# Performance work log

Hardware: AMD Instinct MI355X
Metric: run time of the kernel (lower is better)

Reference implementation:

```python
import jax, jax.numpy as jnp
import numpy as np

B, S, H = 2, 2048, 1024
NH, NKV, HD = 16, 4, 64
E, K, I = 8, 2, 2048
EPS = 1e-6
THETA = 10000.0


def rmsnorm(x, w):
    v = jnp.mean(jnp.square(x.astype(jnp.float32)), axis=-1, keepdims=True)
    return (x.astype(jnp.float32) * jax.lax.rsqrt(v + EPS)).astype(x.dtype) * w


def apply_rope(q, k, pos):
    # q: [B,S,NH,HD], k: [B,S,NKV,HD], pos: [B,S]
    inv_freq = 1.0 / (THETA ** (jnp.arange(0, HD, 2, dtype=jnp.float32) / HD))
    ang = pos.astype(jnp.float32)[..., None] * inv_freq          # [B,S,HD/2]
    emb = jnp.concatenate([ang, ang], axis=-1)                   # [B,S,HD]
    cos = jnp.cos(emb)[:, :, None, :]
    sin = jnp.sin(emb)[:, :, None, :]

    def rot(x):
        return jnp.concatenate([-x[..., HD // 2:], x[..., :HD // 2]], axis=-1)

    q = (q * cos + rot(q) * sin).astype(q.dtype)
    k = (k * cos + rot(k) * sin).astype(k.dtype)
    return q, k


def setup_inputs() -> dict:
    key = jax.random.key(0)
    ks = jax.random.split(key, 10)
    sc = 0.02
    return dict(
        hidden_states=jax.random.normal(ks[0], (B, S, H), jnp.float32),
        attention_mask=jnp.ones((B, S), jnp.int32),
        position_ids=jnp.broadcast_to(jnp.arange(S, dtype=jnp.int32), (B, S)),
        norm1_w=jnp.ones((H,), jnp.float32),
        norm2_w=jnp.ones((H,), jnp.float32),
        wq=jax.random.normal(ks[1], (H, NH * HD), jnp.float32) * sc,
        wk=jax.random.normal(ks[2], (H, NKV * HD), jnp.float32) * sc,
        wv=jax.random.normal(ks[3], (H, NKV * HD), jnp.float32) * sc,
        wo=jax.random.normal(ks[4], (NH * HD, H), jnp.float32) * sc,
        gate_w=jax.random.normal(ks[5], (H, E), jnp.float32) * sc,
        w1=jax.random.normal(ks[6], (E, H, I), jnp.float32) * sc,
        w3=jax.random.normal(ks[7], (E, H, I), jnp.float32) * sc,
        w2=jax.random.normal(ks[8], (E, I, H), jnp.float32) * sc,
    )


def reference(hidden_states, attention_mask, position_ids, norm1_w, norm2_w,
              wq, wk, wv, wo, gate_w, w1, w3, w2):
    x = hidden_states
    # --- attention block ---
    h = rmsnorm(x, norm1_w)
    q = (h @ wq).reshape(B, S, NH, HD)
    k = (h @ wk).reshape(B, S, NKV, HD)
    v = (h @ wv).reshape(B, S, NKV, HD)
    q, k = apply_rope(q, k, position_ids)
    rep = NH // NKV
    k = jnp.repeat(k, rep, axis=2)   # [B,S,NH,HD]
    v = jnp.repeat(v, rep, axis=2)
    q = q.transpose(0, 2, 1, 3)      # [B,NH,S,HD]
    k = k.transpose(0, 2, 1, 3)
    v = v.transpose(0, 2, 1, 3)
    scores = jnp.einsum('bhqd,bhkd->bhqk', q, k) / jnp.sqrt(jnp.float32(HD))
    causal = jnp.tril(jnp.ones((S, S), jnp.bool_))
    mask = causal[None, None, :, :] & (attention_mask[:, None, None, :] > 0)
    neg = jnp.finfo(jnp.float32).min
    scores = jnp.where(mask, scores, neg)
    attn = jax.nn.softmax(scores.astype(jnp.float32), axis=-1).astype(x.dtype)
    o = jnp.einsum('bhqk,bhkd->bhqd', attn, v)
    o = o.transpose(0, 2, 1, 3).reshape(B, S, NH * HD) @ wo
    x = x + o
    # --- MoE block ---
    h = rmsnorm(x, norm2_w)
    router_logits = (h @ gate_w).astype(jnp.float32)            # [B,S,E]
    routing_weights, selected_experts = jax.lax.top_k(router_logits, K)
    routing_weights = jax.nn.softmax(routing_weights, axis=-1)  # [B,S,K]
    moe = jnp.zeros_like(h)
    for e in range(E):
        eo = (jax.nn.silu(h @ w1[e]) * (h @ w3[e])) @ w2[e]     # [B,S,H]
        wgt = jnp.sum((selected_experts == e) * routing_weights, axis=-1)[:, :, None]
        moe = moe + wgt.astype(h.dtype) * eo
    x = x + moe
    return x, router_logits
```

## Files before the change

kernel.cpp:

```cpp
#include <hip/hip_runtime.h>
#include <cstdint>
#include <cstddef>

#define BB 2
#define SS 2048
#define HH 1024
#define NHEADS 16
#define NKVH 4
#define HDIM 64
#define NEXP 8
#define IDIM 2048
#define NTOK (BB*SS)

typedef __bf16 bf16_t;
typedef bf16_t bf16x8 __attribute__((ext_vector_type(8)));
typedef bf16_t bf16x4 __attribute__((ext_vector_type(4)));
typedef float f32x4 __attribute__((ext_vector_type(4)));

static __device__ __forceinline__ void gl16(const void* g, void* l) {
  __builtin_amdgcn_global_load_lds(
      (const __attribute__((address_space(1))) unsigned int*)g,
      (__attribute__((address_space(3))) unsigned int*)l, 16, 0, 0);
}

__global__ __launch_bounds__(256) void transpose_cvt(
    const float* __restrict__ W, bf16_t* __restrict__ WT, int K, int N)
{
  const float* Wm = W + (size_t)blockIdx.z * K * N;
  bf16_t* Tm = WT + (size_t)blockIdx.z * K * N;
  __shared__ float Ls[64][65];
  int tid = threadIdx.x;
  int k0 = blockIdx.y * 64, n0 = blockIdx.x * 64;
  int rr = tid >> 4, cc = (tid & 15) * 4;
  #pragma unroll
  for (int rep = 0; rep < 4; ++rep) {
    float4 vv = *(const float4*)(Wm + (size_t)(k0 + rep*16 + rr) * N + n0 + cc);
    Ls[rep*16 + rr][cc+0] = vv.x;
    Ls[rep*16 + rr][cc+1] = vv.y;
    Ls[rep*16 + rr][cc+2] = vv.z;
    Ls[rep*16 + rr][cc+3] = vv.w;
  }
  __syncthreads();
  int nn = tid >> 2, ks = (tid & 3) * 16;
  bf16x8 o0, o1;
  #pragma unroll
  for (int j = 0; j < 8; ++j) o0[j] = (bf16_t)Ls[ks + j][nn];
  #pragma unroll
  for (int j = 0; j < 8; ++j) o1[j] = (bf16_t)Ls[ks + 8 + j][nn];
  bf16_t* op = Tm + (size_t)(n0 + nn) * K + k0 + ks;
  *(bf16x8*)op = o0;
  *(bf16x8*)(op + 8) = o1;
}

__global__ __launch_bounds__(256) void rmsnorm_kernel(
    const float* __restrict__ x, const float* __restrict__ w,
    float* __restrict__ outf, bf16_t* __restrict__ outb)
{
  int t = blockIdx.x;
  int tid = threadIdx.x;
  float4 v = ((const float4*)(x + (size_t)t * HH))[tid];
  float ss = v.x*v.x + v.y*v.y + v.z*v.z + v.w*v.w;
  #pragma unroll
  for (int off = 32; off > 0; off >>= 1) ss += __shfl_xor(ss, off);
  __shared__ float red[4];
  if ((tid & 63) == 0) red[tid >> 6] = ss;
  __syncthreads();
  float tot = red[0] + red[1] + red[2] + red[3];
  float scale = 1.0f / sqrtf(tot / (float)HH + 1e-6f);
  float4 wv = ((const float4*)w)[tid];
  float4 o;
  o.x = v.x * scale * wv.x;
  o.y = v.y * scale * wv.y;
  o.z = v.z * scale * wv.z;
  o.w = v.w * scale * wv.w;
  if (outf) ((float4*)(outf + (size_t)t * HH))[tid] = o;
  bf16x4 ob4 = { (bf16_t)o.x, (bf16_t)o.y, (bf16_t)o.z, (bf16_t)o.w };
  *(bf16x4*)(outb + (size_t)t * HH + tid*4) = ob4;
}

__global__ __launch_bounds__(256) void gemm_bt(
    const bf16_t* __restrict__ A, const bf16_t* __restrict__ Bt,
    const float* __restrict__ R, float* __restrict__ C, int N, int K)
{
  __shared__ __align__(16) bf16_t As[4096];
  __shared__ __align__(16) bf16_t Bs[4096];
  int tid = threadIdx.x, lane = tid & 63, w = tid >> 6;
  int l4 = lane & 15, g = lane >> 4;
  int m0 = blockIdx.y * 128, n0 = blockIdx.x * 128;
  int lrow = w*16 + (lane >> 2), lk = (lane & 3) * 8;
  const bf16_t* ag0 = A + (size_t)(m0 + lrow) * K + lk;
  const bf16_t* ag1 = ag0 + (size_t)64 * K;
  const bf16_t* bg0 = Bt + (size_t)(n0 + lrow) * K + lk;
  const bf16_t* bg1 = bg0 + (size_t)64 * K;
  bf16_t* lA0 = As + w*512;  bf16_t* lA1 = As + 2048 + w*512;
  bf16_t* lB0 = Bs + w*512;  bf16_t* lB1 = Bs + 2048 + w*512;
  const f32x4 fz = {0.f,0.f,0.f,0.f};
  f32x4 acc[4][4];
  #pragma unroll
  for (int i = 0; i < 4; ++i) { acc[i][0]=fz; acc[i][1]=fz; acc[i][2]=fz; acc[i][3]=fz; }
  int wm = (w >> 1) * 64, wn = (w & 1) * 64;
  for (int k0 = 0; k0 < K; k0 += 32) {
    __syncthreads();
    gl16(ag0, lA0); gl16(ag1, lA1); gl16(bg0, lB0); gl16(bg1, lB1);
    ag0 += 32; ag1 += 32; bg0 += 32; bg1 += 32;
    __syncthreads();
    bf16x8 af[4], bfr[4];
    #pragma unroll
    for (int mi = 0; mi < 4; ++mi) af[mi] = *(const bf16x8*)&As[(wm + mi*16 + l4)*32 + g*8];
    #pragma unroll
    for (int ni = 0; ni < 4; ++ni) bfr[ni] = *(const bf16x8*)&Bs[(wn + ni*16 + l4)*32 + g*8];
    #pragma unroll
    for (int mi = 0; mi < 4; ++mi)
      #pragma unroll
      for (int ni = 0; ni < 4; ++ni)
        acc[mi][ni] = __builtin_amdgcn_mfma_f32_16x16x32_bf16(af[mi], bfr[ni], acc[mi][ni], 0, 0, 0);
  }
  #pragma unroll
  for (int mi = 0; mi < 4; ++mi) {
    int rowb = m0 + wm + mi*16 + g*4;
    #pragma unroll
    for (int r = 0; r < 4; ++r) {
      size_t rb = (size_t)(rowb + r) * N;
      #pragma unroll
      for (int ni = 0; ni < 4; ++ni) {
        int col = n0 + wn + ni*16 + l4;
        float vv = acc[mi][ni][r];
        C[rb + col] = R ? vv + R[rb + col] : vv;
      }
    }
  }
}

__global__ __launch_bounds__(256) void rope_kernel(
    float* __restrict__ q, float* __restrict__ k, const int* __restrict__ pos_ids)
{
  int idx = blockIdx.x * 256 + threadIdx.x;
  int token = idx / 640;
  int rem = idx - token * 640;
  int head = rem >> 5;
  int i = rem & 31;
  float pos = (float)pos_ids[token];
  float inv = __expf(-(float)i * (9.210340371976184f / 32.0f));
  float ang = pos * inv;
  float s, c;
  sincosf(ang, &s, &c);
  float* p;
  if (head < NHEADS) p = q + (size_t)token * (NHEADS*HDIM) + head * HDIM;
  else               p = k + (size_t)token * (NKVH*HDIM) + (head - NHEADS) * HDIM;
  float x1 = p[i], x2 = p[i + 32];
  p[i]      = x1 * c - x2 * s;
  p[i + 32] = x2 * c + x1 * s;
}

__global__ __launch_bounds__(256) void attn_mfma_kernel(
    const float* __restrict__ q, const float* __restrict__ k, const float* __restrict__ v,
    const int* __restrict__ amask, bf16_t* __restrict__ out)
{
  __shared__ bf16_t Khi[64][72];
  __shared__ bf16_t Klo[64][72];
  __shared__ bf16_t Vhi[64][72];
  __shared__ bf16_t Vlo[64][72];
  __shared__ bf16_t Phi[4][16][72];
  __shared__ bf16_t Plo[4][16][72];
  __shared__ float ms[64];
  int tid = threadIdx.x, lane = tid & 63, w = tid >> 6;
  int l4 = lane & 15, g = lane >> 4;
  int bh = blockIdx.y;
  int b = bh >> 4, h = bh & 15, kvh = h >> 2;
  int qb = gridDim.x - 1 - blockIdx.x;
  int r0 = qb * 64;

  bf16x8 qh[2], ql[2];
  {
    const float* qp = q + (size_t)(b*SS + r0 + w*16 + l4) * (NHEADS*HDIM) + h*HDIM + g*8;
    #pragma unroll
    for (int st = 0; st < 2; ++st) {
      float4 t0 = *(const float4*)(qp + st*32);
      float4 t1 = *(const float4*)(qp + st*32 + 4);
      float f[8] = {t0.x*0.125f, t0.y*0.125f, t0.z*0.125f, t0.w*0.125f,
                    t1.x*0.125f, t1.y*0.125f, t1.z*0.125f, t1.w*0.125f};
      #pragma unroll
      for (int j = 0; j < 8; ++j) {
        bf16_t hi = (bf16_t)f[j];
        qh[st][j] = hi;
        ql[st][j] = (bf16_t)(f[j] - (float)hi);
      }
    }
  }
  const f32x4 fz = {0.f,0.f,0.f,0.f};
  f32x4 o[4]; o[0]=fz; o[1]=fz; o[2]=fz; o[3]=fz;
  float mrow[4] = {-3e38f,-3e38f,-3e38f,-3e38f};
  float lrow[4] = {0.f,0.f,0.f,0.f};

  int vkey = tid & 63;
  int dvb = (tid >> 6) * 16;
  int nch = qb + 1;
  for (int ch = 0; ch < nch; ++ch) {
    int kc = ch * 64;
    __syncthreads();
    #pragma unroll
    for (int it = 0; it < 4; ++it) {
      int slot = it*256 + tid;
      int key = slot >> 4, dq = (slot & 15) * 4;
      float4 kk4 = *(const float4*)(k + (size_t)(b*SS + kc + key)*(NKVH*HDIM) + kvh*HDIM + dq);
      bf16_t kh0 = (bf16_t)kk4.x, kh1 = (bf16_t)kk4.y, kh2 = (bf16_t)kk4.z, kh3 = (bf16_t)kk4.w;
      bf16x4 khv = {kh0, kh1, kh2, kh3};
      bf16x4 klv = { (bf16_t)(kk4.x-(float)kh0), (bf16_t)(kk4.y-(float)kh1),
                     (bf16_t)(kk4.z-(float)kh2), (bf16_t)(kk4.w-(float)kh3) };
      *(bf16x4*)&Khi[key][dq] = khv;
      *(bf16x4*)&Klo[key][dq] = klv;
      int dv = dvb + it*4;
      float4 vv4 = *(const float4*)(v + (size_t)(b*SS + kc + vkey)*(NKVH*HDIM) + kvh*HDIM + dv);
      float vf4[4] = {vv4.x, vv4.y, vv4.z, vv4.w};
      #pragma unroll
      for (int j = 0; j < 4; ++j) {
        bf16_t hi = (bf16_t)vf4[j];
        Vhi[dv+j][vkey] = hi;
        Vlo[dv+j][vkey] = (bf16_t)(vf4[j] - (float)hi);
      }
    }
    if (tid < 64) ms[tid] = (amask[b*SS + kc + tid] > 0) ? 0.f : -3e38f;
    __syncthreads();
    f32x4 s[4]; s[0]=fz; s[1]=fz; s[2]=fz; s[3]=fz;
    #pragma unroll
    for (int st = 0; st < 2; ++st) {
      #pragma unroll
      for (int c = 0; c < 4; ++c) {
        bf16x8 kfh = *(const bf16x8*)&Khi[c*16 + l4][st*32 + g*8];
        bf16x8 kfl = *(const bf16x8*)&Klo[c*16 + l4][st*32 + g*8];
        s[c] = __builtin_amdgcn_mfma_f32_16x16x32_bf16(qh[st], kfh, s[c], 0, 0, 0);
        s[c] = __builtin_amdgcn_mfma_f32_16x16x32_bf16(qh[st], kfl, s[c], 0, 0, 0);
        s[c] = __builtin_amdgcn_mfma_f32_16x16x32_bf16(ql[st], kfh, s[c], 0, 0, 0);
      }
    }
    #pragma unroll
    for (int c = 0; c < 4; ++c) {
      int kg = kc + c*16 + l4;
      float mk = ms[c*16 + l4];
      #pragma unroll
      for (int r = 0; r < 4; ++r) {
        int rowg = r0 + w*16 + g*4 + r;
        float sv = s[c][r] + mk;
        s[c][r] = (kg <= rowg) ? sv : -3e38f;
      }
    }
    float mnew[4], alpha[4];
    #pragma unroll
    for (int r = 0; r < 4; ++r) {
      float mc = fmaxf(fmaxf(s[0][r], s[1][r]), fmaxf(s[2][r], s[3][r]));
      mc = fmaxf(mc, __shfl_xor(mc, 1));
      mc = fmaxf(mc, __shfl_xor(mc, 2));
      mc = fmaxf(mc, __shfl_xor(mc, 4));
      mc = fmaxf(mc, __shfl_xor(mc, 8));
      mnew[r] = fmaxf(mrow[r], mc);
      alpha[r] = __expf(mrow[r] - mnew[r]);
      mrow[r] = mnew[r];
    }
    float rsum[4] = {0.f,0.f,0.f,0.f};
    #pragma unroll
    for (int c = 0; c < 4; ++c) {
      #pragma unroll
      for (int r = 0; r < 4; ++r) {
        float p = __expf(s[c][r] - mnew[r]);
        s[c][r] = p;
        rsum[r] += p;
      }
    }
    #pragma unroll
    for (int r = 0; r < 4; ++r) {
      float t = rsum[r];
      t += __shfl_xor(t, 1); t += __shfl_xor(t, 2);
      t += __shfl_xor(t, 4); t += __shfl_xor(t, 8);
      lrow[r] = lrow[r] * alpha[r] + t;
      o[0][r] *= alpha[r]; o[1][r] *= alpha[r]; o[2][r] *= alpha[r]; o[3][r] *= alpha[r];
    }
    #pragma unroll
    for (int c = 0; c < 4; ++c) {
      #pragma unroll
      for (int r = 0; r < 4; ++r) {
        float p = s[c][r];
        bf16_t hi = (bf16_t)p;
        Phi[w][g*4 + r][c*16 + l4] = hi;
        Plo[w][g*4 + r][c*16 + l4] = (bf16_t)(p - (float)hi);
      }
    }
    __syncthreads();
    #pragma unroll
    for (int st = 0; st < 2; ++st) {
      bf16x8 pfh = *(const bf16x8*)&Phi[w][l4][st*32 + g*8];
      bf16x8 pfl = *(const bf16x8*)&Plo[w][l4][st*32 + g*8];
      #pragma unroll
      for (int c = 0; c < 4; ++c) {
        bf16x8 vfh = *(const bf16x8*)&Vhi[c*16 + l4][st*32 + g*8];
        bf16x8 vfl = *(const bf16x8*)&Vlo[c*16 + l4][st*32 + g*8];
        o[c] = __builtin_amdgcn_mfma_f32_16x16x32_bf16(pfh, vfh, o[c], 0, 0, 0);
        o[c] = __builtin_amdgcn_mfma_f32_16x16x32_bf16(pfl, vfh, o[c], 0, 0, 0);
        o[c] = __builtin_amdgcn_mfma_f32_16x16x32_bf16(pfh, vfl, o[c], 0, 0, 0);
      }
    }
  }
  #pragma unroll
  for (int r = 0; r < 4; ++r) {
    float inv = (lrow[r] > 0.f) ? 1.f / lrow[r] : 0.f;
    int row = r0 + w*16 + g*4 + r;
    bf16_t* op = out + (size_t)(b*SS + row) * (NHEADS*HDIM) + h*HDIM;
    #pragma unroll
    for (int c = 0; c < 4; ++c)
      op[c*16 + l4] = (bf16_t)(o[c][r] * inv);
  }
}

__global__ __launch_bounds__(256) void router_kernel(
    const float* __restrict__ h2, const float* __restrict__ gw,
    float* __restrict__ logits_out, int* __restrict__ sel, float* __restrict__ wts,
    int* __restrict__ counts)
{
  int tid = threadIdx.x, lane = tid & 63, w = tid >> 6;
  int tok = blockIdx.x * 4 + w;
  float acc[NEXP] = {0.f,0.f,0.f,0.f,0.f,0.f,0.f,0.f};
  const float* xr = h2 + (size_t)tok * HH;
  for (int hh = lane; hh < HH; hh += 64) {
    float xv = xr[hh];
    const float* gr = gw + (size_t)hh * NEXP;
    #pragma unroll
    for (int e = 0; e < NEXP; ++e) acc[e] += xv * gr[e];
  }
  #pragma unroll
  for (int e = 0; e < NEXP; ++e) {
    #pragma unroll
    for (int off = 32; off > 0; off >>= 1) acc[e] += __shfl_xor(acc[e], off);
  }
  if (lane == 0) {
    float* lo = logits_out + (size_t)tok * NEXP;
    #pragma unroll
    for (int e = 0; e < NEXP; ++e) lo[e] = acc[e];
    int b0 = 0; float v0 = acc[0];
    #pragma unroll
    for (int e = 1; e < NEXP; ++e) if (acc[e] > v0) { v0 = acc[e]; b0 = e; }
    int b1 = -1; float v1 = -1e38f;
    #pragma unroll
    for (int e = 0; e < NEXP; ++e) if (e != b0 && acc[e] > v1) { v1 = acc[e]; b1 = e; }
    float wa = 1.f / (1.f + __expf(v1 - v0));
    sel[tok*2] = b0; sel[tok*2+1] = b1;
    wts[tok*2] = wa; wts[tok*2+1] = 1.f - wa;
    atomicAdd(&counts[b0], 1);
    atomicAdd(&counts[b1], 1);
  }
}

__global__ void scan_kernel(const int* __restrict__ counts, int* __restrict__ offsets,
                            int* __restrict__ fill)
{
  if (threadIdx.x == 0 && blockIdx.x == 0) {
    int o = 0;
    for (int e = 0; e < NEXP; ++e) { offsets[e] = o; o += counts[e]; fill[e] = 0; }
  }
}

__global__ __launch_bounds__(256) void scatter_kernel(
    const int* __restrict__ sel, const int* __restrict__ offsets, int* __restrict__ fill,
    int* __restrict__ etok, int* __restrict__ tslot)
{
  int t = blockIdx.x * 256 + threadIdx.x;
  if (t >= NTOK) return;
  #pragma unroll
  for (int s = 0; s < 2; ++s) {
    int e = sel[t*2 + s];
    int p = atomicAdd(&fill[e], 1);
    int slot = offsets[e] + p;
    etok[slot] = t;
    tslot[t*2 + s] = slot;
  }
}

__global__ __launch_bounds__(256) void moe_mm1(
    const bf16_t* __restrict__ hb, const bf16_t* __restrict__ w1t,
    const int* __restrict__ counts, const int* __restrict__ offsets,
    const int* __restrict__ etok, bf16_t* __restrict__ G)
{
  int e = blockIdx.z, cnt = counts[e], mb = blockIdx.y;
  if (mb * 128 >= cnt) return;
  int off = offsets[e];
  __shared__ __align__(16) bf16_t As[4096];
  __shared__ __align__(16) bf16_t Bs[4096];
  int tid = threadIdx.x, lane = tid & 63, w = tid >> 6;
  int l4 = lane & 15, g = lane >> 4;
  int n0 = blockIdx.x * 128;
  int lrow = w*16 + (lane >> 2), lk = (lane & 3) * 8;
  int r0 = mb*128 + lrow, r1 = r0 + 64;
  int t0 = etok[off + (r0 < cnt ? r0 : cnt-1)];
  int t1 = etok[off + (r1 < cnt ? r1 : cnt-1)];
  const bf16_t* ag0 = hb + (size_t)t0 * HH + lk;
  const bf16_t* ag1 = hb + (size_t)t1 * HH + lk;
  const bf16_t* Bt = w1t + (size_t)e * IDIM * HH;
  const bf16_t* bg0 = Bt + (size_t)(n0 + lrow) * HH + lk;
  const bf16_t* bg1 = bg0 + (size_t)64 * HH;
  bf16_t* lA0 = As + w*512;  bf16_t* lA1 = As + 2048 + w*512;
  bf16_t* lB0 = Bs + w*512;  bf16_t* lB1 = Bs + 2048 + w*512;
  const f32x4 fz = {0.f,0.f,0.f,0.f};
  f32x4 acc[4][4];
  #pragma unroll
  for (int i = 0; i < 4; ++i) { acc[i][0]=fz; acc[i][1]=fz; acc[i][2]=fz; acc[i][3]=fz; }
  int wm = (w >> 1) * 64, wn = (w & 1) * 64;
  for (int k0 = 0; k0 < HH; k0 += 32) {
    __syncthreads();
    gl16(ag0, lA0); gl16(ag1, lA1); gl16(bg0, lB0); gl16(bg1, lB1);
    ag0 += 32; ag1 += 32; bg0 += 32; bg1 += 32;
    __syncthreads();
    bf16x8 af[4], bfr[4];
    #pragma unroll
    for (int mi = 0; mi < 4; ++mi) af[mi] = *(const bf16x8*)&As[(wm + mi*16 + l4)*32 + g*8];
    #pragma unroll
    for (int ni = 0; ni < 4; ++ni) bfr[ni] = *(const bf16x8*)&Bs[(wn + ni*16 + l4)*32 + g*8];
    #pragma unroll
    for (int mi = 0; mi < 4; ++mi)
      #pragma unroll
      for (int ni = 0; ni < 4; ++ni)
        acc[mi][ni] = __builtin_amdgcn_mfma_f32_16x16x32_bf16(af[mi], bfr[ni], acc[mi][ni], 0, 0, 0);
  }
  #pragma unroll
  for (int mi = 0; mi < 4; ++mi) {
    #pragma unroll
    for (int r = 0; r < 4; ++r) {
      int slot = mb*128 + wm + mi*16 + g*4 + r;
      if (slot < cnt) {
        size_t rb = (size_t)(off + slot) * IDIM;
        #pragma unroll
        for (int ni = 0; ni < 4; ++ni)
          G[rb + n0 + wn + ni*16 + l4] = (bf16_t)acc[mi][ni][r];
      }
    }
  }
}

__global__ __launch_bounds__(256) void moe_mm3(
    const bf16_t* __restrict__ hb, const bf16_t* __restrict__ w3t,
    const int* __restrict__ counts, const int* __restrict__ offsets,
    const int* __restrict__ etok, bf16_t* __restrict__ G)
{
  int e = blockIdx.z, cnt = counts[e], mb = blockIdx.y;
  if (mb * 128 >= cnt) return;
  int off = offsets[e];
  __shared__ __align__(16) bf16_t As[4096];
  __shared__ __align__(16) bf16_t Bs[4096];
  int tid = threadIdx.x, lane = tid & 63, w = tid >> 6;
  int l4 = lane & 15, g = lane >> 4;
  int n0 = blockIdx.x * 128;
  int lrow = w*16 + (lane >> 2), lk = (lane & 3) * 8;
  int r0 = mb*128 + lrow, r1 = r0 + 64;
  int t0 = etok[off + (r0 < cnt ? r0 : cnt-1)];
  int t1 = etok[off + (r1 < cnt ? r1 : cnt-1)];
  const bf16_t* ag0 = hb + (size_t)t0 * HH + lk;
  const bf16_t* ag1 = hb + (size_t)t1 * HH + lk;
  const bf16_t* Bt = w3t + (size_t)e * IDIM * HH;
  const bf16_t* bg0 = Bt + (size_t)(n0 + lrow) * HH + lk;
  const bf16_t* bg1 = bg0 + (size_t)64 * HH;
  bf16_t* lA0 = As + w*512;  bf16_t* lA1 = As + 2048 + w*512;
  bf16_t* lB0 = Bs + w*512;  bf16_t* lB1 = Bs + 2048 + w*512;
  const f32x4 fz = {0.f,0.f,0.f,0.f};
  f32x4 acc[4][4];
  #pragma unroll
  for (int i = 0; i < 4; ++i) { acc[i][0]=fz; acc[i][1]=fz; acc[i][2]=fz; acc[i][3]=fz; }
  int wm = (w >> 1) * 64, wn = (w & 1) * 64;
  for (int k0 = 0; k0 < HH; k0 += 32) {
    __syncthreads();
    gl16(ag0, lA0); gl16(ag1, lA1); gl16(bg0, lB0); gl16(bg1, lB1);
    ag0 += 32; ag1 += 32; bg0 += 32; bg1 += 32;
    __syncthreads();
    bf16x8 af[4], bfr[4];
    #pragma unroll
    for (int mi = 0; mi < 4; ++mi) af[mi] = *(const bf16x8*)&As[(wm + mi*16 + l4)*32 + g*8];
    #pragma unroll
    for (int ni = 0; ni < 4; ++ni) bfr[ni] = *(const bf16x8*)&Bs[(wn + ni*16 + l4)*32 + g*8];
    #pragma unroll
    for (int mi = 0; mi < 4; ++mi)
      #pragma unroll
      for (int ni = 0; ni < 4; ++ni)
        acc[mi][ni] = __builtin_amdgcn_mfma_f32_16x16x32_bf16(af[mi], bfr[ni], acc[mi][ni], 0, 0, 0);
  }
  #pragma unroll
  for (int mi = 0; mi < 4; ++mi) {
    #pragma unroll
    for (int r = 0; r < 4; ++r) {
      int slot = mb*128 + wm + mi*16 + g*4 + r;
      if (slot < cnt) {
        size_t rb = (size_t)(off + slot) * IDIM;
        #pragma unroll
        for (int ni = 0; ni < 4; ++ni) {
          size_t idx = rb + n0 + wn + ni*16 + l4;
          float gv = (float)G[idx];
          float sv = gv / (1.f + __expf(-gv));
          G[idx] = (bf16_t)(sv * acc[mi][ni][r]);
        }
      }
    }
  }
}

__global__ __launch_bounds__(256) void moe_mm2(
    const bf16_t* __restrict__ act, const bf16_t* __restrict__ w2t,
    const int* __restrict__ counts, const int* __restrict__ offsets,
    float* __restrict__ eo)
{
  int e = blockIdx.z, cnt = counts[e], mb = blockIdx.y;
  if (mb * 128 >= cnt) return;
  int off = offsets[e];
  __shared__ __align__(16) bf16_t As[4096];
  __shared__ __align__(16) bf16_t Bs[4096];
  int tid = threadIdx.x, lane = tid & 63, w = tid >> 6;
  int l4 = lane & 15, g = lane >> 4;
  int n0 = blockIdx.x * 128;
  int lrow = w*16 + (lane >> 2), lk = (lane & 3) * 8;
  int r0 = mb*128 + lrow, r1 = r0 + 64;
  int cr0 = (r0 < cnt ? r0 : cnt-1), cr1 = (r1 < cnt ? r1 : cnt-1);
  const bf16_t* ag0 = act + (size_t)(off + cr0) * IDIM + lk;
  const bf16_t* ag1 = act + (size_t)(off + cr1) * IDIM + lk;
  const bf16_t* Bt = w2t + (size_t)e * HH * IDIM;
  const bf16_t* bg0 = Bt + (size_t)(n0 + lrow) * IDIM + lk;
  const bf16_t* bg1 = bg0 + (size_t)64 * IDIM;
  bf16_t* lA0 = As + w*512;  bf16_t* lA1 = As + 2048 + w*512;
  bf16_t* lB0 = Bs + w*512;  bf16_t* lB1 = Bs + 2048 + w*512;
  const f32x4 fz = {0.f,0.f,0.f,0.f};
  f32x4 acc[4][4];
  #pragma unroll
  for (int i = 0; i < 4; ++i) { acc[i][0]=fz; acc[i][1]=fz; acc[i][2]=fz; acc[i][3]=fz; }
  int wm = (w >> 1) * 64, wn = (w & 1) * 64;
  for (int k0 = 0; k0 < IDIM; k0 += 32) {
    __syncthreads();
    gl16(ag0, lA0); gl16(ag1, lA1); gl16(bg0, lB0); gl16(bg1, lB1);
    ag0 += 32; ag1 += 32; bg0 += 32; bg1 += 32;
    __syncthreads();
    bf16x8 af[4], bfr[4];
    #pragma unroll
    for (int mi = 0; mi < 4; ++mi) af[mi] = *(const bf16x8*)&As[(wm + mi*16 + l4)*32 + g*8];
    #pragma unroll
    for (int ni = 0; ni < 4; ++ni) bfr[ni] = *(const bf16x8*)&Bs[(wn + ni*16 + l4)*32 + g*8];
    #pragma unroll
    for (int mi = 0; mi < 4; ++mi)
      #pragma unroll
      for (int ni = 0; ni < 4; ++ni)
        acc[mi][ni] = __builtin_amdgcn_mfma_f32_16x16x32_bf16(af[mi], bfr[ni], acc[mi][ni], 0, 0, 0);
  }
  #pragma unroll
  for (int mi = 0; mi < 4; ++mi) {
    #pragma unroll
    for (int r = 0; r < 4; ++r) {
      int slot = mb*128 + wm + mi*16 + g*4 + r;
      if (slot < cnt) {
        size_t rb = (size_t)(off + slot) * HH;
        #pragma unroll
        for (int ni = 0; ni < 4; ++ni)
          eo[rb + n0 + wn + ni*16 + l4] = acc[mi][ni][r];
      }
    }
  }
}

__global__ __launch_bounds__(256) void combine_kernel(
    const float* __restrict__ eo, const int* __restrict__ tslot,
    const float* __restrict__ wts, float* __restrict__ out)
{
  int t = blockIdx.x;
  int c = threadIdx.x * 4;
  int s0 = tslot[t*2], s1 = tslot[t*2 + 1];
  float w0 = wts[t*2], w1 = wts[t*2 + 1];
  float4 o = *(float4*)(out + (size_t)t * HH + c);
  float4 a = *(const float4*)(eo + (size_t)s0 * HH + c);
  float4 b = *(const float4*)(eo + (size_t)s1 * HH + c);
  o.x += w0*a.x + w1*b.x;
  o.y += w0*a.y + w1*b.y;
  o.z += w0*a.z + w1*b.z;
  o.w += w0*a.w + w1*b.w;
  *(float4*)(out + (size_t)t * HH + c) = o;
}

extern "C" void kernel_launch(void* const* d_in, const int* in_sizes, int n_in,
                              void* d_out, int out_size, void* d_ws, size_t ws_size,
                              hipStream_t stream)
{
  const float* x    = (const float*)d_in[0];
  const int*   am   = (const int*)d_in[1];
  const int*   pid  = (const int*)d_in[2];
  const float* n1w  = (const float*)d_in[3];
  const float* n2w  = (const float*)d_in[4];
  const float* wq   = (const float*)d_in[5];
  const float* wk   = (const float*)d_in[6];
  const float* wv   = (const float*)d_in[7];
  const float* wo   = (const float*)d_in[8];
  const float* gw   = (const float*)d_in[9];
  const float* w1   = (const float*)d_in[10];
  const float* w3   = (const float*)d_in[11];
  const float* w2   = (const float*)d_in[12];
  float* out = (float*)d_out;
  float* rlogits = out + (size_t)NTOK * HH;

  char* base = (char*)d_ws;
  bf16_t* hb  = (bf16_t*)(base);
  float*  h2  = (float*)(base + (8ull<<20));
  float*  qb  = (float*)(base + (24ull<<20));
  float*  kb  = (float*)(base + (40ull<<20));
  float*  vb  = (float*)(base + (44ull<<20));
  bf16_t* ob  = (bf16_t*)(base + (48ull<<20));
  bf16_t* G   = (bf16_t*)(base + (24ull<<20));
  float*  eo  = (float*)(base + (56ull<<20));
  bf16_t* wqt = (bf16_t*)(base + (88ull<<20));
  bf16_t* wkt = (bf16_t*)(base + (90ull<<20));
  bf16_t* wvt = (bf16_t*)(base + (90ull<<20) + (512ull<<10));
  bf16_t* wot = (bf16_t*)(base + (91ull<<20));
  bf16_t* w1t = (bf16_t*)(base + (93ull<<20));
  bf16_t* w3t = (bf16_t*)(base + (125ull<<20));
  bf16_t* w2t = (bf16_t*)(base + (157ull<<20));
  char* sm = base + (189ull<<20);
  int*   sel   = (int*)sm;
  float* wts   = (float*)(sm + (64<<10));
  int*   etok  = (int*)(sm + (128<<10));
  int*   tslot = (int*)(sm + (192<<10));
  int* counts  = (int*)(sm + (256<<10));
  int* offsets = counts + 8;
  int* fill    = counts + 16;

  transpose_cvt<<<dim3(16,16,1), 256, 0, stream>>>(wq, wqt, 1024, 1024);
  transpose_cvt<<<dim3(4,16,1),  256, 0, stream>>>(wk, wkt, 1024, 256);
  transpose_cvt<<<dim3(4,16,1),  256, 0, stream>>>(wv, wvt, 1024, 256);
  transpose_cvt<<<dim3(16,16,1), 256, 0, stream>>>(wo, wot, 1024, 1024);
  transpose_cvt<<<dim3(32,16,8), 256, 0, stream>>>(w1, w1t, 1024, 2048);
  transpose_cvt<<<dim3(32,16,8), 256, 0, stream>>>(w3, w3t, 1024, 2048);
  transpose_cvt<<<dim3(16,32,8), 256, 0, stream>>>(w2, w2t, 2048, 1024);
  hipMemsetAsync(counts, 0, 3 * 8 * sizeof(int), stream);

  rmsnorm_kernel<<<NTOK, 256, 0, stream>>>(x, n1w, nullptr, hb);
  gemm_bt<<<dim3(8,32),  256, 0, stream>>>(hb, wqt, nullptr, qb, NHEADS*HDIM, HH);
  gemm_bt<<<dim3(2,32),  256, 0, stream>>>(hb, wkt, nullptr, kb, NKVH*HDIM, HH);
  gemm_bt<<<dim3(2,32),  256, 0, stream>>>(hb, wvt, nullptr, vb, NKVH*HDIM, HH);
  rope_kernel<<<(NTOK*640)/256, 256, 0, stream>>>(qb, kb, pid);
  attn_mfma_kernel<<<dim3(SS/64, BB*NHEADS), 256, 0, stream>>>(qb, kb, vb, am, ob);
  gemm_bt<<<dim3(8,32),  256, 0, stream>>>(ob, wot, x, out, HH, NHEADS*HDIM);

  rmsnorm_kernel<<<NTOK, 256, 0, stream>>>(out, n2w, h2, hb);
  router_kernel<<<NTOK/4, 256, 0, stream>>>(h2, gw, rlogits, sel, wts, counts);
  scan_kernel<<<1, 64, 0, stream>>>(counts, offsets, fill);
  scatter_kernel<<<NTOK/256, 256, 0, stream>>>(sel, offsets, fill, etok, tslot);
  moe_mm1<<<dim3(16,32,8), 256, 0, stream>>>(hb, w1t, counts, offsets, etok, G);
  moe_mm3<<<dim3(16,32,8), 256, 0, stream>>>(hb, w3t, counts, offsets, etok, G);
  moe_mm2<<<dim3(8,32,8),  256, 0, stream>>>(G, w2t, counts, offsets, eo);
  combine_kernel<<<NTOK, 256, 0, stream>>>(eo, tslot, wts, out);
}
```

Before: 1.026 ms.

## Pre-pack K/V into swizzled bf16 hi/lo and use 128-row query tiles

A new pack_kv kernel converts K and V once into split bf16 hi/lo arrays, with V transposed and XOR-swizzled. The attention kernel can then load them straight into LDS with global_load_lds rather than converting them per block. Each attention block now covers 128 query rows across two 64-row sub-tiles, so every K/V chunk in LDS is reused twice. Fully masked causal sub-tiles are skipped, and launch bounds request 3 blocks per CU. The cost is an extra kernel launch, more registers per thread and fewer blocks in the grid. The __syncthreads between the P writes and P reads is also gone, since each wave uses only its own P buffer.

```diff
diff --git a/kernel.cpp b/kernel.cpp
--- a/kernel.cpp
+++ b/kernel.cpp
@@ -152,27 +152,78 @@
   p[i + 32] = x2 * c + x1 * s;
 }
 
-__global__ __launch_bounds__(256) void attn_mfma_kernel(
-    const float* __restrict__ q, const float* __restrict__ k, const float* __restrict__ v,
+__global__ __launch_bounds__(256) void pack_kv(
+    const float* __restrict__ kb, const float* __restrict__ vb,
+    bf16_t* __restrict__ Khig, bf16_t* __restrict__ Klog,
+    bf16_t* __restrict__ Vhig, bf16_t* __restrict__ Vlog)
+{
+  __shared__ float Ls[64][68];
+  int ch = blockIdx.x, bk = blockIdx.y;
+  int b = bk >> 2, kvh = bk & 3;
+  int tid = threadIdx.x;
+  int key = tid >> 2, d0 = (tid & 3) * 16;
+  size_t src = ((size_t)(b*SS + ch*64 + key) * NKVH + kvh) * HDIM + d0;
+  float f[16];
+  *(float4*)(f)     = *(const float4*)(kb + src);
+  *(float4*)(f+4)   = *(const float4*)(kb + src + 4);
+  *(float4*)(f+8)   = *(const float4*)(kb + src + 8);
+  *(float4*)(f+12)  = *(const float4*)(kb + src + 12);
+  size_t krow = ((size_t)bk*SS + ch*64 + key) * 64;
+  int sw = key & 7, j0 = d0 >> 3;
+  bf16x8 hi0, lo0, hi1, lo1;
+  #pragma unroll
+  for (int j = 0; j < 8; ++j) {
+    bf16_t h = (bf16_t)f[j];     hi0[j] = h; lo0[j] = (bf16_t)(f[j]   - (float)h);
+    bf16_t h2 = (bf16_t)f[8+j];  hi1[j] = h2; lo1[j] = (bf16_t)(f[8+j] - (float)h2);
+  }
+  *(bf16x8*)&Khig[krow + ((j0 ^ sw) << 3)]       = hi0;
+  *(bf16x8*)&Khig[krow + (((j0+1) ^ sw) << 3)]   = hi1;
+  *(bf16x8*)&Klog[krow + ((j0 ^ sw) << 3)]       = lo0;
+  *(bf16x8*)&Klog[krow + (((j0+1) ^ sw) << 3)]   = lo1;
+  *(float4*)&Ls[key][d0]      = *(const float4*)(vb + src);
+  *(float4*)&Ls[key][d0 + 4]  = *(const float4*)(vb + src + 4);
+  *(float4*)&Ls[key][d0 + 8]  = *(const float4*)(vb + src + 8);
+  *(float4*)&Ls[key][d0 + 12] = *(const float4*)(vb + src + 12);
+  __syncthreads();
+  int d = tid >> 2, k0 = (tid & 3) * 16;
+  size_t vrow = ((size_t)(bk*32 + ch) * 64 + d) * 64;
+  int swv = d & 7;
+  #pragma unroll
+  for (int half = 0; half < 2; ++half) {
+    bf16x8 vh, vl;
+    #pragma unroll
+    for (int j = 0; j < 8; ++j) {
+      float x = Ls[k0 + half*8 + j][d];
+      bf16_t h = (bf16_t)x;
+      vh[j] = h; vl[j] = (bf16_t)(x - (float)h);
+    }
+    int jj = (k0 >> 3) + half;
+    *(bf16x8*)&Vhig[vrow + ((jj ^ swv) << 3)] = vh;
+    *(bf16x8*)&Vlog[vrow + ((jj ^ swv) << 3)] = vl;
+  }
+}
+
+__global__ __launch_bounds__(256, 3) void attn_mfma_kernel(
+    const float* __restrict__ q,
+    const bf16_t* __restrict__ Khig, const bf16_t* __restrict__ Klog,
+    const bf16_t* __restrict__ Vhig, const bf16_t* __restrict__ Vlog,
     const int* __restrict__ amask, bf16_t* __restrict__ out)
 {
-  __shared__ bf16_t Khi[64][72];
-  __shared__ bf16_t Klo[64][72];
-  __shared__ bf16_t Vhi[64][72];
-  __shared__ bf16_t Vlo[64][72];
-  __shared__ bf16_t Phi[4][16][72];
-  __shared__ bf16_t Plo[4][16][72];
+  __shared__ __align__(16) bf16_t Khi[4096], Klo[4096], Vhi[4096], Vlo[4096];
+  __shared__ bf16_t Phi[4][16][72], Plo[4][16][72];
   __shared__ float ms[64];
   int tid = threadIdx.x, lane = tid & 63, w = tid >> 6;
   int l4 = lane & 15, g = lane >> 4;
   int bh = blockIdx.y;
   int b = bh >> 4, h = bh & 15, kvh = h >> 2;
+  int bk = b * NKVH + kvh;
   int qb = gridDim.x - 1 - blockIdx.x;
-  int r0 = qb * 64;
-
-  bf16x8 qh[2], ql[2];
-  {
-    const float* qp = q + (size_t)(b*SS + r0 + w*16 + l4) * (NHEADS*HDIM) + h*HDIM + g*8;
+  int r0 = qb * 128;
+
+  bf16x8 qh[2][2], ql[2][2];
+  #pragma unroll
+  for (int mi = 0; mi < 2; ++mi) {
+    const float* qp = q + (size_t)(b*SS + r0 + mi*64 + w*16 + l4) * (NHEADS*HDIM) + h*HDIM + g*8;
     #pragma unroll
     for (int st = 0; st < 2; ++st) {
       float4 t0 = *(const float4*)(qp + st*32);
@@ -182,131 +233,137 @@
       #pragma unroll
       for (int j = 0; j < 8; ++j) {
         bf16_t hi = (bf16_t)f[j];
-        qh[st][j] = hi;
-        ql[st][j] = (bf16_t)(f[j] - (float)hi);
+        qh[mi][st][j] = hi;
+        ql[mi][st][j] = (bf16_t)(f[j] - (float)hi);
       }
     }
   }
   const f32x4 fz = {0.f,0.f,0.f,0.f};
-  f32x4 o[4]; o[0]=fz; o[1]=fz; o[2]=fz; o[3]=fz;
-  float mrow[4] = {-3e38f,-3e38f,-3e38f,-3e38f};
-  float lrow[4] = {0.f,0.f,0.f,0.f};
-
-  int vkey = tid & 63;
-  int dvb = (tid >> 6) * 16;
-  int nch = qb + 1;
+  f32x4 o[2][4];
+  float mrow[2][4], lrow[2][4];
+  #pragma unroll
+  for (int mi = 0; mi < 2; ++mi)
+    #pragma unroll
+    for (int c = 0; c < 4; ++c) { o[mi][c] = fz; mrow[mi][c] = -3e38f; lrow[mi][c] = 0.f; }
+
+  const bf16_t* Khb = Khig + (size_t)bk*SS*64;
+  const bf16_t* Klb = Klog + (size_t)bk*SS*64;
+  const bf16_t* Vhb = Vhig + (size_t)bk*SS*64;
+  const bf16_t* Vlb = Vlog + (size_t)bk*SS*64;
+  int nch = 2*qb + 2;
   for (int ch = 0; ch < nch; ++ch) {
     int kc = ch * 64;
     __syncthreads();
-    #pragma unroll
-    for (int it = 0; it < 4; ++it) {
-      int slot = it*256 + tid;
-      int key = slot >> 4, dq = (slot & 15) * 4;
-      float4 kk4 = *(const float4*)(k + (size_t)(b*SS + kc + key)*(NKVH*HDIM) + kvh*HDIM + dq);
-      bf16_t kh0 = (bf16_t)kk4.x, kh1 = (bf16_t)kk4.y, kh2 = (bf16_t)kk4.z, kh3 = (bf16_t)kk4.w;
-      bf16x4 khv = {kh0, kh1, kh2, kh3};
-      bf16x4 klv = { (bf16_t)(kk4.x-(float)kh0), (bf16_t)(kk4.y-(float)kh1),
-                     (bf16_t)(kk4.z-(float)kh2), (bf16_t)(kk4.w-(float)kh3) };
-      *(bf16x4*)&Khi[key][dq] = khv;
-      *(bf16x4*)&Klo[key][dq] = klv;
-      int dv = dvb + it*4;
-      float4 vv4 = *(const float4*)(v + (size_t)(b*SS + kc + vkey)*(NKVH*HDIM) + kvh*HDIM + dv);
-      float vf4[4] = {vv4.x, vv4.y, vv4.z, vv4.w};
-      #pragma unroll
-      for (int j = 0; j < 4; ++j) {
-        bf16_t hi = (bf16_t)vf4[j];
-        Vhi[dv+j][vkey] = hi;
-        Vlo[dv+j][vkey] = (bf16_t)(vf4[j] - (float)hi);
-      }
+    {
+      size_t ko = (size_t)(kc + w*16) * 64 + lane*8;
+      gl16(Khb + ko,       Khi + w*1024);
+      gl16(Khb + ko + 512, Khi + w*1024 + 512);
+      gl16(Klb + ko,       Klo + w*1024);
+      gl16(Klb + ko + 512, Klo + w*1024 + 512);
+      size_t vo = (size_t)ch*4096 + (size_t)(w*16)*64 + lane*8;
+      gl16(Vhb + vo,       Vhi + w*1024);
+      gl16(Vhb + vo + 512, Vhi + w*1024 + 512);
+      gl16(Vlb + vo,       Vlo + w*1024);
+      gl16(Vlb + vo + 512, Vlo + w*1024 + 512);
     }
     if (tid < 64) ms[tid] = (amask[b*SS + kc + tid] > 0) ? 0.f : -3e38f;
     __syncthreads();
-    f32x4 s[4]; s[0]=fz; s[1]=fz; s[2]=fz; s[3]=fz;
-    #pragma unroll
-    for (int st = 0; st < 2; ++st) {
+    #pragma unroll
+    for (int mi = 0; mi < 2; ++mi) {
+      int tbase = r0 + mi*64 + w*16;
+      if (kc > tbase + 15) continue;
+      f32x4 s[4]; s[0]=fz; s[1]=fz; s[2]=fz; s[3]=fz;
+      #pragma unroll
+      for (int st = 0; st < 2; ++st) {
+        #pragma unroll
+        for (int c = 0; c < 4; ++c) {
+          int po = (c*16 + l4)*64 + (((st*4 + g) ^ (l4 & 7)) << 3);
+          bf16x8 kfh = *(const bf16x8*)&Khi[po];
+          bf16x8 kfl = *(const bf16x8*)&Klo[po];
+          s[c] = __builtin_amdgcn_mfma_f32_16x16x32_bf16(qh[mi][st], kfh, s[c], 0, 0, 0);
+          s[c] = __builtin_amdgcn_mfma_f32_16x16x32_bf16(qh[mi][st], kfl, s[c], 0, 0, 0);
+          s[c] = __builtin_amdgcn_mfma_f32_16x16x32_bf16(ql[mi][st], kfh, s[c], 0, 0, 0);
+        }
+      }
       #pragma unroll
       for (int c = 0; c < 4; ++c) {
-        bf16x8 kfh = *(const bf16x8*)&Khi[c*16 + l4][st*32 + g*8];
-        bf16x8 kfl = *(const bf16x8*)&Klo[c*16 + l4][st*32 + g*8];
-        s[c] = __builtin_amdgcn_mfma_f32_16x16x32_bf16(qh[st], kfh, s[c], 0, 0, 0);
-        s[c] = __builtin_amdgcn_mfma_f32_16x16x32_bf16(qh[st], kfl, s[c], 0, 0, 0);
-        s[c] = __builtin_amdgcn_mfma_f32_16x16x32_bf16(ql[st], kfh, s[c], 0, 0, 0);
-      }
-    }
-    #pragma unroll
-    for (int c = 0; c < 4; ++c) {
-      int kg = kc + c*16 + l4;
-      float mk = ms[c*16 + l4];
+        int kg = kc + c*16 + l4;
+        float mk = ms[c*16 + l4];
+        #pragma unroll
+        for (int r = 0; r < 4; ++r) {
+          int rowg = tbase + g*4 + r;
+          float sv = s[c][r] + mk;
+          s[c][r] = (kg <= rowg) ? sv : -3e38f;
+        }
+      }
+      float mnew[4], alpha[4];
       #pragma unroll
       for (int r = 0; r < 4; ++r) {
-        int rowg = r0 + w*16 + g*4 + r;
-        float sv = s[c][r] + mk;
-        s[c][r] = (kg <= rowg) ? sv : -3e38f;
-      }
-    }
-    float mnew[4], alpha[4];
+        float mc = fmaxf(fmaxf(s[0][r], s[1][r]), fmaxf(s[2][r], s[3][r]));
+        mc = fmaxf(mc, __shfl_xor(mc, 1));
+        mc = fmaxf(mc, __shfl_xor(mc, 2));
+        mc = fmaxf(mc, __shfl_xor(mc, 4));
+        mc = fmaxf(mc, __shfl_xor(mc, 8));
+        mnew[r] = fmaxf(mrow[mi][r], mc);
+        alpha[r] = __expf(mrow[mi][r] - mnew[r]);
+        mrow[mi][r] = mnew[r];
+      }
+      float rsum[4] = {0.f,0.f,0.f,0.f};
+      #pragma unroll
+      for (int c = 0; c < 4; ++c) {
+        #pragma unroll
+        for (int r = 0; r < 4; ++r) {
+          float p = __expf(s[c][r] - mnew[r]);
+          s[c][r] = p;
+          rsum[r] += p;
+        }
+      }
+      #pragma unroll
+      for (int r = 0; r < 4; ++r) {
+        float t = rsum[r];
+        t += __shfl_xor(t, 1); t += __shfl_xor(t, 2);
+        t += __shfl_xor(t, 4); t += __shfl_xor(t, 8);
+        lrow[mi][r] = lrow[mi][r] * alpha[r] + t;
+        o[mi][0][r] *= alpha[r]; o[mi][1][r] *= alpha[r];
+        o[mi][2][r] *= alpha[r]; o[mi][3][r] *= alpha[r];
+      }
+      #pragma unroll
+      for (int c = 0; c < 4; ++c) {
+        #pragma unroll
+        for (int r = 0; r < 4; ++r) {
+          float p = s[c][r];
+          bf16_t hi = (bf16_t)p;
+          Phi[w][g*4 + r][c*16 + l4] = hi;
+          Plo[w][g*4 + r][c*16 + l4] = (bf16_t)(p - (float)hi);
+        }
+      }
+      #pragma unroll
+      for (int st = 0; st < 2; ++st) {
+        bf16x8 pfh = *(const bf16x8*)&Phi[w][l4][st*32 + g*8];
+        bf16x8 pfl = *(const bf16x8*)&Plo[w][l4][st*32 + g*8];
+        #pragma unroll
+        for (int c = 0; c < 4; ++c) {
+          int po = (c*16 + l4)*64 + (((st*4 + g) ^ (l4 & 7)) << 3);
+          bf16x8 vfh = *(const bf16x8*)&Vhi[po];
+          bf16x8 vfl = *(const bf16x8*)&Vlo[po];
+          o[mi][c] = __builtin_amdgcn_mfma_f32_16x16x32_bf16(pfh, vfh, o[mi][c], 0, 0, 0);
+          o[mi][c] = __builtin_amdgcn_mfma_f32_16x16x32_bf16(pfl, vfh, o[mi][c], 0, 0, 0);
+          o[mi][c] = __builtin_amdgcn_mfma_f32_16x16x32_bf16(pfh, vfl, o[mi][c], 0, 0, 0);
+        }
+      }
+    }
+  }
+  #pragma unroll
+  for (int mi = 0; mi < 2; ++mi) {
     #pragma unroll
     for (int r = 0; r < 4; ++r) {
-      float mc = fmaxf(fmaxf(s[0][r], s[1][r]), fmaxf(s[2][r], s[3][r]));
-      mc = fmaxf(mc, __shfl_xor(mc, 1));
-      mc = fmaxf(mc, __shfl_xor(mc, 2));
-      mc = fmaxf(mc, __shfl_xor(mc, 4));
-      mc = fmaxf(mc, __shfl_xor(mc, 8));
-      mnew[r] = fmaxf(mrow[r], mc);
-      alpha[r] = __expf(mrow[r] - mnew[r]);
-      mrow[r] = mnew[r];
-    }
-    float rsum[4] = {0.f,0.f,0.f,0.f};
-    #pragma unroll
-    for (int c = 0; c < 4; ++c) {
-      #pragma unroll
-      for (int r = 0; r < 4; ++r) {
-        float p = __expf(s[c][r] - mnew[r]);
-        s[c][r] = p;
-        rsum[r] += p;
-      }
-    }
-    #pragma unroll
-    for (int r = 0; r < 4; ++r) {
-      float t = rsum[r];
-      t += __shfl_xor(t, 1); t += __shfl_xor(t, 2);
-      t += __shfl_xor(t, 4); t += __shfl_xor(t, 8);
-      lrow[r] = lrow[r] * alpha[r] + t;
-      o[0][r] *= alpha[r]; o[1][r] *= alpha[r]; o[2][r] *= alpha[r]; o[3][r] *= alpha[r];
-    }
-    #pragma unroll
-    for (int c = 0; c < 4; ++c) {
-      #pragma unroll
-      for (int r = 0; r < 4; ++r) {
-        float p = s[c][r];
-        bf16_t hi = (bf16_t)p;
-        Phi[w][g*4 + r][c*16 + l4] = hi;
-        Plo[w][g*4 + r][c*16 + l4] = (bf16_t)(p - (float)hi);
-      }
-    }
-    __syncthreads();
-    #pragma unroll
-    for (int st = 0; st < 2; ++st) {
-      bf16x8 pfh = *(const bf16x8*)&Phi[w][l4][st*32 + g*8];
-      bf16x8 pfl = *(const bf16x8*)&Plo[w][l4][st*32 + g*8];
-      #pragma unroll
-      for (int c = 0; c < 4; ++c) {
-        bf16x8 vfh = *(const bf16x8*)&Vhi[c*16 + l4][st*32 + g*8];
-        bf16x8 vfl = *(const bf16x8*)&Vlo[c*16 + l4][st*32 + g*8];
-        o[c] = __builtin_amdgcn_mfma_f32_16x16x32_bf16(pfh, vfh, o[c], 0, 0, 0);
-        o[c] = __builtin_amdgcn_mfma_f32_16x16x32_bf16(pfl, vfh, o[c], 0, 0, 0);
-        o[c] = __builtin_amdgcn_mfma_f32_16x16x32_bf16(pfh, vfl, o[c], 0, 0, 0);
-      }
-    }
-  }
-  #pragma unroll
-  for (int r = 0; r < 4; ++r) {
-    float inv = (lrow[r] > 0.f) ? 1.f / lrow[r] : 0.f;
-    int row = r0 + w*16 + g*4 + r;
-    bf16_t* op = out + (size_t)(b*SS + row) * (NHEADS*HDIM) + h*HDIM;
-    #pragma unroll
-    for (int c = 0; c < 4; ++c)
-      op[c*16 + l4] = (bf16_t)(o[c][r] * inv);
+      float inv = (lrow[mi][r] > 0.f) ? 1.f / lrow[mi][r] : 0.f;
+      int row = r0 + mi*64 + w*16 + g*4 + r;
+      bf16_t* op = out + (size_t)(b*SS + row) * (NHEADS*HDIM) + h*HDIM;
+      #pragma unroll
+      for (int c = 0; c < 4; ++c)
+        op[c*16 + l4] = (bf16_t)(o[mi][c][r] * inv);
+    }
   }
 }
 
@@ -603,6 +660,10 @@
   bf16_t* ob  = (bf16_t*)(base + (48ull<<20));
   bf16_t* G   = (bf16_t*)(base + (24ull<<20));
   float*  eo  = (float*)(base + (56ull<<20));
+  bf16_t* Khig = (bf16_t*)(base + (56ull<<20));
+  bf16_t* Klog = (bf16_t*)(base + (58ull<<20));
+  bf16_t* Vhig = (bf16_t*)(base + (60ull<<20));
+  bf16_t* Vlog = (bf16_t*)(base + (62ull<<20));
   bf16_t* wqt = (bf16_t*)(base + (88ull<<20));
   bf16_t* wkt = (bf16_t*)(base + (90ull<<20));
   bf16_t* wvt = (bf16_t*)(base + (90ull<<20) + (512ull<<10));
@@ -633,7 +694,8 @@
   gemm_bt<<<dim3(2,32),  256, 0, stream>>>(hb, wkt, nullptr, kb, NKVH*HDIM, HH);
   gemm_bt<<<dim3(2,32),  256, 0, stream>>>(hb, wvt, nullptr, vb, NKVH*HDIM, HH);
   rope_kernel<<<(NTOK*640)/256, 256, 0, stream>>>(qb, kb, pid);
-  attn_mfma_kernel<<<dim3(SS/64, BB*NHEADS), 256, 0, stream>>>(qb, kb, vb, am, ob);
+  pack_kv<<<dim3(32, BB*NKVH), 256, 0, stream>>>(kb, vb, Khig, Klog, Vhig, Vlog);
+  attn_mfma_kernel<<<dim3(SS/128, BB*NHEADS), 256, 0, stream>>>(qb, Khig, Klog, Vhig, Vlog, am, ob);
   gemm_bt<<<dim3(8,32),  256, 0, stream>>>(ob, wot, x, out, HH, NHEADS*HDIM);
 
   rmsnorm_kernel<<<NTOK, 256, 0, stream>>>(out, n2w, h2, hb);
```

After: 981.7 us. 4.3% less time.
